# Performance work log

Hardware: AMD Instinct MI355X
Metric: run time of the kernel (lower is better)

## Reference

```python
import jax, jax.numpy as jnp
import numpy as np
from jax import lax

GRID_SIZE = 5
SPLINE_ORDER = 3
N_COEF = GRID_SIZE + SPLINE_ORDER  # 8 b-spline basis functions per input
GRID_LO, GRID_HI = -1.0, 1.0


def _grid():
    h = (GRID_HI - GRID_LO) / GRID_SIZE
    return jnp.arange(-SPLINE_ORDER, GRID_SIZE + SPLINE_ORDER + 1, dtype=jnp.float32) * h + GRID_LO


def _bsplines(x):
    # x: [..., in] -> [..., in, N_COEF] via Cox-de Boor recursion (efficient-kan)
    grid = _grid()
    x = x[..., None]
    bases = ((x >= grid[:-1]) & (x < grid[1:])).astype(x.dtype)
    for j in range(1, SPLINE_ORDER + 1):
        bases = ((x - grid[:-(j + 1)]) / (grid[j:-1] - grid[:-(j + 1)]) * bases[..., :-1]
                 + (grid[j + 1:] - x) / (grid[j + 1:] - grid[1:-j]) * bases[..., 1:])
    return bases


def _kan_linear(x, base_w, spline_w):
    # x: [..., in]; base_w: [out, in]; spline_w: [out, in, N_COEF]
    base = jax.nn.silu(x) @ base_w.T
    b = _bsplines(x).reshape(x.shape[:-1] + (-1,))  # [..., in*N_COEF]
    return base + b @ spline_w.reshape(spline_w.shape[0], -1).T


def _kan_conv(x, base_w, spline_w):
    # x: [B, C, H, W]; 3x3 valid KAN convolution
    patches = lax.conv_general_dilated_patches(x, (3, 3), (1, 1), 'VALID')  # [B, C*9, H-2, W-2]
    p = patches.transpose(0, 2, 3, 1)  # [B, Ho, Wo, C*9]
    out = _kan_linear(p, base_w, spline_w)  # [B, Ho, Wo, out]
    return out.transpose(0, 3, 1, 2)


def _maxpool2(x):
    return lax.reduce_window(x, -jnp.inf, lax.max, (1, 1, 2, 2), (1, 1, 2, 2), 'VALID')


def setup_inputs() -> dict:
    key = jax.random.key(0)
    ks = jax.random.split(key, 12)
    B = 2048
    x = jax.random.uniform(ks[0], (B, 1, 28, 28), dtype=jnp.float32)
    s = 0.1
    return {
        'x': x,
        'bw1': jax.random.normal(ks[1], (5, 9), dtype=jnp.float32) * s,
        'sw1': jax.random.normal(ks[2], (5, 9, N_COEF), dtype=jnp.float32) * s,
        'bw2': jax.random.normal(ks[3], (5, 45), dtype=jnp.float32) * s,
        'sw2': jax.random.normal(ks[4], (5, 45, N_COEF), dtype=jnp.float32) * s,
        'bw3': jax.random.normal(ks[5], (2, 45), dtype=jnp.float32) * s,
        'sw3': jax.random.normal(ks[6], (2, 45, N_COEF), dtype=jnp.float32) * s,
        'w1': jax.random.normal(ks[7], (500, 162), dtype=jnp.float32) * 0.05,
        'b1': jnp.zeros((500,), dtype=jnp.float32),
        'w2': jax.random.normal(ks[8], (10, 500), dtype=jnp.float32) * 0.05,
        'b2': jnp.zeros((10,), dtype=jnp.float32),
    }


def reference(x, bw1, sw1, bw2, sw2, bw3, sw3, w1, b1, w2, b2):
    h = _kan_conv(x, bw1, sw1)       # [B, 5, 26, 26]
    h = _maxpool2(h)                 # [B, 5, 13, 13]
    h = _kan_conv(h, bw2, sw2)       # [B, 5, 11, 11]
    h = _kan_conv(h, bw3, sw3)       # [B, 2, 9, 9]
    h = h.reshape(h.shape[0], -1)    # [B, 162]
    h = jax.nn.relu(h @ w1.T + b1)   # [B, 500]
    return h @ w2.T + b2             # [B, 10]
```

## Files before the change

### kernel.cpp

```cpp
#include <hip/hip_runtime.h>


typedef _Float16 h2 __attribute__((ext_vector_type(2)));

__device__ __forceinline__ h2 u2h(unsigned int u) {
  union { unsigned int x; h2 h; } v; v.x = u; return v.h;
}
__device__ __forceinline__ unsigned short f2h_bits(float x) {
  union { _Float16 h; unsigned short u; } v; v.h = (_Float16)x; return v.u;
}
__device__ __forceinline__ float h2f(unsigned short u) {
  union { unsigned short u; _Float16 h; } v; v.u = u; return (float)v.h;
}
__device__ __forceinline__ unsigned int pack2h(float a, float b) {
  return (unsigned int)f2h_bits(a) | ((unsigned int)f2h_bits(b) << 16);
}
__device__ __forceinline__ float fdot2(h2 a, h2 b, float c) {
  return __builtin_amdgcn_fdot2(a, b, c, false);
}

__device__ __forceinline__ void featurize_regs(float v, uint4& bs, float& silu) {
  silu = v / (1.0f + __expf(-v));
  bs.x = 0u; bs.y = 0u; bs.z = 0u; bs.w = 0u;
  float u = fmaf(v, 2.5f, 5.5f);
  if (u >= 0.0f && u < 11.0f) {
    float tf = floorf(u);
    float f = u - tf, f2 = f * f, f3 = f2 * f, om = 1.0f - f;
    const float c6 = 1.0f / 6.0f;
    float w0 = om * om * om * c6;
    float w1 = (3.0f * f3 - 6.0f * f2 + 4.0f) * c6;
    float w2 = (-3.0f * f3 + 3.0f * f2 + 3.0f * f + 1.0f) * c6;
    float w3 = f3 * c6;
    unsigned long long w01 =
        (unsigned long long)f2h_bits(w0) |
        ((unsigned long long)f2h_bits(w1) << 16) |
        ((unsigned long long)f2h_bits(w2) << 32) |
        ((unsigned long long)f2h_bits(w3) << 48);
    int t = (int)tf;
    int s = 16 * t - 48;
    unsigned long long lo, hi;
    if (s >= 0) {
      lo = (s < 64) ? (w01 << s) : 0ull;
      hi = (s == 0) ? 0ull : ((s < 64) ? (w01 >> (64 - s)) : (w01 << (s - 64)));
    } else {
      lo = w01 >> (-s);
      hi = 0ull;
    }
    bs.x = (unsigned int)lo; bs.y = (unsigned int)(lo >> 32);
    bs.z = (unsigned int)hi; bs.w = (unsigned int)(hi >> 32);
  }
}

__global__ __launch_bounds__(256) void k_prep(
    const float* __restrict__ bw1, const float* __restrict__ sw1,
    const float* __restrict__ bw2, const float* __restrict__ sw2,
    const float* __restrict__ bw3, const float* __restrict__ sw3,
    const float* __restrict__ w1, const float* __restrict__ w2,
    unsigned int* __restrict__ V1s, float* __restrict__ V1b,
    unsigned int* __restrict__ V2s, float* __restrict__ V2b,
    unsigned int* __restrict__ V3s, float* __restrict__ V3b,
    unsigned int* __restrict__ W1p4, float* __restrict__ W2p) {
  int t = blockIdx.x * 256 + threadIdx.x;
  if (t < 180) {
    int p = t & 3, o = (t >> 2) % 5, in = t / 20;
    V1s[t] = pack2h(sw1[(o * 9 + in) * 8 + 2 * p], sw1[(o * 9 + in) * 8 + 2 * p + 1]);
  }
  if (t < 45)  { int o = t % 5, in = t / 5; V1b[t] = bw1[o * 9 + in]; }
  if (t < 900) {
    int p = t & 3, o = (t >> 2) % 5, in = t / 20;
    V2s[t] = pack2h(sw2[(o * 45 + in) * 8 + 2 * p], sw2[(o * 45 + in) * 8 + 2 * p + 1]);
  }
  if (t < 225) { int o = t % 5, in = t / 5; V2b[t] = bw2[o * 45 + in]; }
  if (t < 360) {
    int p = t & 3, o = (t >> 2) & 1, in = t / 8;
    V3s[t] = pack2h(sw3[(o * 45 + in) * 8 + 2 * p], sw3[(o * 45 + in) * 8 + 2 * p + 1]);
  }
  if (t < 90)  { int o = t % 2, in = t / 2; V3b[t] = bw3[o * 45 + in]; }
  if (t < 43008) {
    int j = t & 3, o = (t >> 2) & 511, g = t >> 11;
    int kp = g * 4 + j;
    W1p4[t] = (o < 500 && kp < 81)
                  ? pack2h(w1[o * 162 + 2 * kp], w1[o * 162 + 2 * kp + 1])
                  : 0u;
  }
  if (t < 5120) {
    int o = t >> 9, k = t & 511;
    W2p[t] = (k < 500) ? w2[o * 500 + k] : 0.0f;
  }
}

__global__ __launch_bounds__(128, 4) void k_fused(
    const float* __restrict__ x,
    const unsigned int* __restrict__ V1s, const float* __restrict__ V1b,
    const unsigned int* __restrict__ V2s, const float* __restrict__ V2b,
    const unsigned int* __restrict__ V3s, const float* __restrict__ V3b,
    const unsigned int* __restrict__ W1p4, const float* __restrict__ W2p,
    const float* __restrict__ b1, const float* __restrict__ b2,
    float* __restrict__ out) {
  __shared__ uint4 bas[845];
  __shared__ unsigned short slu16[848];
  __shared__ float red[20];
  float*        basF = (float*)bas;
  float*        h3f  = basF + 2048;
  unsigned int* hpk  = (unsigned int*)basF + 2560;
  const int b = blockIdx.x;
  const int tid = threadIdx.x;

  #pragma unroll 1
  for (int l = tid; l < 784; l += 128) {
    uint4 bs; float sl;
    featurize_regs(x[b * 784 + l], bs, sl);
    bas[l] = bs; slu16[l] = f2h_bits(sl);
  }
  __syncthreads();

  float h1v[2][5];
  #pragma unroll 1
  for (int it = 0; it < 2; ++it) {
    int p = it * 128 + tid;
    if (p < 169) {
      int py = p / 13, px = p % 13;
      int r0 = py * 2, c0 = px * 2;
      float wacc[4][5];
      #pragma unroll
      for (int wi = 0; wi < 4; ++wi)
        #pragma unroll
        for (int o = 0; o < 5; ++o) wacc[wi][o] = 0.0f;
      #pragma unroll
      for (int r = 0; r < 4; ++r) {
        uint4 q[4]; float sl[4];
        #pragma unroll
        for (int c = 0; c < 4; ++c) {
          q[c]  = bas[(r0 + r) * 28 + c0 + c];
          sl[c] = h2f(slu16[(r0 + r) * 28 + c0 + c]);
        }
        #pragma unroll
        for (int c = 0; c < 4; ++c) {
          h2 a0 = u2h(q[c].x), a1 = u2h(q[c].y), a2 = u2h(q[c].z), a3 = u2h(q[c].w);
          #pragma unroll
          for (int dy = 0; dy < 2; ++dy) {
            #pragma unroll
            for (int dx = 0; dx < 2; ++dx) {
              int ky = r - dy, kx = c - dx;
              if (ky >= 0 && ky < 3 && kx >= 0 && kx < 3) {
                const unsigned int* wp = V1s + (ky * 3 + kx) * 20;
                const float* bp = V1b + (ky * 3 + kx) * 5;
                #pragma unroll
                for (int o = 0; o < 5; ++o) {
                  float acc = wacc[dy * 2 + dx][o];
                  acc = fdot2(a0, u2h(wp[o * 4 + 0]), acc);
                  acc = fdot2(a1, u2h(wp[o * 4 + 1]), acc);
                  acc = fdot2(a2, u2h(wp[o * 4 + 2]), acc);
                  acc = fdot2(a3, u2h(wp[o * 4 + 3]), acc);
                  wacc[dy * 2 + dx][o] = fmaf(sl[c], bp[o], acc);
                }
              }
            }
          }
        }
      }
      #pragma unroll
      for (int o = 0; o < 5; ++o)
        h1v[it][o] = fmaxf(fmaxf(wacc[0][o], wacc[1][o]),
                           fmaxf(wacc[2][o], wacc[3][o]));
    }
  }
  __syncthreads();
  #pragma unroll 1
  for (int it = 0; it < 2; ++it) {
    int p = it * 128 + tid;
    if (p < 169) {
      #pragma unroll
      for (int o = 0; o < 5; ++o) {
        uint4 bs; float sl;
        featurize_regs(h1v[it][o], bs, sl);
        bas[o * 169 + p] = bs; slu16[o * 169 + p] = f2h_bits(sl);
      }
    }
  }
  __syncthreads();

  float acc2[5];
  {
    #pragma unroll
    for (int o = 0; o < 5; ++o) acc2[o] = 0.0f;
    int pc = (tid < 121) ? tid : 120;
    int y0 = pc / 11, x0 = pc % 11;
    #pragma unroll 1
    for (int cky = 0; cky < 15; ++cky) {
      int c = cky / 3, ky = cky - c * 3;
      int ba0 = c * 169 + (y0 + ky) * 13 + x0;
      uint4 q00 = bas[ba0], q01 = bas[ba0 + 1], q02 = bas[ba0 + 2];
      float s00 = h2f(slu16[ba0]), s01 = h2f(slu16[ba0 + 1]), s02 = h2f(slu16[ba0 + 2]);
      uint4 wq[15]; float wb[15];
      const uint4* wp4 = (const uint4*)(V2s + cky * 60);
      const float* bp  = V2b + cky * 15;
      #pragma unroll
      for (int i = 0; i < 15; ++i) { wq[i] = wp4[i]; wb[i] = bp[i]; }
      #pragma unroll
      for (int kx = 0; kx < 3; ++kx) {
        uint4 q = (kx == 0) ? q00 : ((kx == 1) ? q01 : q02);
        float sl = (kx == 0) ? s00 : ((kx == 1) ? s01 : s02);
        h2 a0 = u2h(q.x), a1 = u2h(q.y), a2 = u2h(q.z), a3 = u2h(q.w);
        #pragma unroll
        for (int o = 0; o < 5; ++o) {
          uint4 w = wq[kx * 5 + o];
          float a = acc2[o];
          a = fdot2(a0, u2h(w.x), a);
          a = fdot2(a1, u2h(w.y), a);
          a = fdot2(a2, u2h(w.z), a);
          a = fdot2(a3, u2h(w.w), a);
          acc2[o] = fmaf(sl, wb[kx * 5 + o], a);
        }
      }
    }
  }
  __syncthreads();
  if (tid < 121) {
    #pragma unroll
    for (int o = 0; o < 5; ++o) {
      uint4 bs; float sl;
      featurize_regs(acc2[o], bs, sl);
      bas[o * 121 + tid] = bs; slu16[o * 121 + tid] = f2h_bits(sl);
    }
  }
  __syncthreads();

  float acc3[2];
  {
    acc3[0] = acc3[1] = 0.0f;
    int pc = (tid < 81) ? tid : 80;
    int y0 = pc / 9, x0 = pc % 9;
    #pragma unroll 1
    for (int cky = 0; cky < 15; ++cky) {
      int c = cky / 3, ky = cky - c * 3;
      int ba0 = c * 121 + (y0 + ky) * 11 + x0;
      uint4 q00 = bas[ba0], q01 = bas[ba0 + 1], q02 = bas[ba0 + 2];
      float s00 = h2f(slu16[ba0]), s01 = h2f(slu16[ba0 + 1]), s02 = h2f(slu16[ba0 + 2]);
      uint4 wq[6]; float wb[6];
      const uint4* wp4 = (const uint4*)(V3s + cky * 24);
      const float* bp  = V3b + cky * 6;
      #pragma unroll
      for (int i = 0; i < 6; ++i) { wq[i] = wp4[i]; wb[i] = bp[i]; }
      #pragma unroll
      for (int kx = 0; kx < 3; ++kx) {
        uint4 q = (kx == 0) ? q00 : ((kx == 1) ? q01 : q02);
        float sl = (kx == 0) ? s00 : ((kx == 1) ? s01 : s02);
        h2 a0 = u2h(q.x), a1 = u2h(q.y), a2 = u2h(q.z), a3 = u2h(q.w);
        #pragma unroll
        for (int o = 0; o < 2; ++o) {
          uint4 w = wq[kx * 2 + o];
          float a = acc3[o];
          a = fdot2(a0, u2h(w.x), a);
          a = fdot2(a1, u2h(w.y), a);
          a = fdot2(a2, u2h(w.z), a);
          a = fdot2(a3, u2h(w.w), a);
          acc3[o] = fmaf(sl, wb[kx * 2 + o], a);
        }
      }
    }
  }
  __syncthreads();
  if (tid < 81) { h3f[tid] = acc3[0]; h3f[81 + tid] = acc3[1]; }
  __syncthreads();
  if (tid < 84)
    hpk[tid] = (tid < 81) ? pack2h(h3f[2 * tid], h3f[2 * tid + 1]) : 0u;
  __syncthreads();

  float fa[4];
  #pragma unroll
  for (int i = 0; i < 4; ++i) fa[i] = 0.0f;
  {
    const uint4* hp4 = (const uint4*)hpk;
    const uint4* wbase = (const uint4*)W1p4 + tid;
    uint4 wA[4], wB[4];
    #pragma unroll
    for (int i = 0; i < 4; ++i) wA[i] = wbase[i * 128];
    #pragma unroll 1
    for (int g = 0; g < 21; g += 2) {
      if (g + 1 < 21) {
        const uint4* p = wbase + (g + 1) * 512;
        #pragma unroll
        for (int i = 0; i < 4; ++i) wB[i] = p[i * 128];
      }
      {
        uint4 hk = hp4[g];
        #pragma unroll
        for (int i = 0; i < 4; ++i) {
          float a = fa[i];
          a = fdot2(u2h(hk.x), u2h(wA[i].x), a);
          a = fdot2(u2h(hk.y), u2h(wA[i].y), a);
          a = fdot2(u2h(hk.z), u2h(wA[i].z), a);
          a = fdot2(u2h(hk.w), u2h(wA[i].w), a);
          fa[i] = a;
        }
      }
      if (g + 2 < 21) {
        const uint4* p = wbase + (g + 2) * 512;
        #pragma unroll
        for (int i = 0; i < 4; ++i) wA[i] = p[i * 128];
      }
      if (g + 1 < 21) {
        uint4 hk = hp4[g + 1];
        #pragma unroll
        for (int i = 0; i < 4; ++i) {
          float a = fa[i];
          a = fdot2(u2h(hk.x), u2h(wB[i].x), a);
          a = fdot2(u2h(hk.y), u2h(wB[i].y), a);
          a = fdot2(u2h(hk.z), u2h(wB[i].z), a);
          a = fdot2(u2h(hk.w), u2h(wB[i].w), a);
          fa[i] = a;
        }
      }
    }
  }
  #pragma unroll
  for (int i = 0; i < 4; ++i) {
    int o = tid + 128 * i;
    float bb = (o < 500) ? b1[o] : 0.0f;
    float v = fa[i] + bb;
    basF[o] = (v > 0.0f && o < 500) ? v : 0.0f;
  }
  __syncthreads();

  float acc10[10];
  {
    float4 ha = ((const float4*)basF)[tid];
    #pragma unroll
    for (int o = 0; o < 10; ++o) {
      const float4* wp = (const float4*)&W2p[o * 512 + 4 * tid];
      float4 w = wp[0];
      acc10[o] = ha.x * w.x + ha.y * w.y + ha.z * w.z + ha.w * w.w;
    }
  }
  #pragma unroll
  for (int off = 32; off > 0; off >>= 1) {
    #pragma unroll
    for (int o = 0; o < 10; ++o) acc10[o] += __shfl_down(acc10[o], off);
  }
  if ((tid & 63) == 0) {
    int wid = tid >> 6;
    #pragma unroll
    for (int o = 0; o < 10; ++o) red[wid * 10 + o] = acc10[o];
  }
  __syncthreads();
  if (tid < 10) out[b * 10 + tid] = red[tid] + red[10 + tid] + b2[tid];
}

extern "C" void kernel_launch(void* const* d_in, const int* in_sizes, int n_in,
                              void* d_out, int out_size, void* d_ws, size_t ws_size,
                              hipStream_t stream) {
  (void)in_sizes; (void)n_in; (void)out_size; (void)ws_size;
  const float* x   = (const float*)d_in[0];
  const float* bw1 = (const float*)d_in[1];
  const float* sw1 = (const float*)d_in[2];
  const float* bw2 = (const float*)d_in[3];
  const float* sw2 = (const float*)d_in[4];
  const float* bw3 = (const float*)d_in[5];
  const float* sw3 = (const float*)d_in[6];
  const float* w1  = (const float*)d_in[7];
  const float* b1  = (const float*)d_in[8];
  const float* w2  = (const float*)d_in[9];
  const float* b2  = (const float*)d_in[10];
  float* out = (float*)d_out;

  char* ws = (char*)d_ws;
  unsigned int* V1s  = (unsigned int*)(ws);
  float*        V1b  = (float*)(ws + 768);
  unsigned int* V2s  = (unsigned int*)(ws + 1024);
  float*        V2b  = (float*)(ws + 4672);
  unsigned int* V3s  = (unsigned int*)(ws + 5632);
  float*        V3b  = (float*)(ws + 7168);
  float*        W2p  = (float*)(ws + 7680);
  unsigned int* W1p4 = (unsigned int*)(ws + 28672);

  k_prep<<<168, 256, 0, stream>>>(bw1, sw1, bw2, sw2, bw3, sw3, w1, w2,
                                  V1s, V1b, V2s, V2b, V3s, V3b, W1p4, W2p);
  k_fused<<<2048, 128, 0, stream>>>(x, V1s, V1b, V2s, V2b, V3s, V3b,
                                    W1p4, W2p, b1, b2, out);
}
```

Baseline: 127.9 us.

## Double block size to 256 threads and split output channels across wave halves

Raises the fused per-sample block from 128 to 256 threads. Conv1 now gives each of the 169 pooled positions its own thread instead of looping twice. In conv2 and conv3 the two 128-thread halves split the output channels (3/2 for conv2, 1/1 for conv3), and the dense layers spread the 512 outputs and the final reduction over 4 waves. The aim is shorter per-thread serial chains and more parallel work per sample. In exchange, more threads sit idle in tail phases and launch bounds are tightened to 256x8, which may pressure registers.

```diff
diff --git a/kernel.cpp b/kernel.cpp
--- a/kernel.cpp
+++ b/kernel.cpp
@@ -51,6 +51,46 @@
   }
 }
 
+template <int OB, int NO>
+__device__ __forceinline__ void conv2_accum(
+    const uint4* bas, const unsigned short* slu16,
+    const unsigned int* __restrict__ V2s, const float* __restrict__ V2b,
+    int y0, int x0, float (&acc)[NO]) {
+  #pragma unroll 1
+  for (int cky = 0; cky < 15; ++cky) {
+    int c = cky / 3, ky = cky - c * 3;
+    int ba0 = c * 169 + (y0 + ky) * 13 + x0;
+    uint4 q00 = bas[ba0], q01 = bas[ba0 + 1], q02 = bas[ba0 + 2];
+    float s00 = h2f(slu16[ba0]), s01 = h2f(slu16[ba0 + 1]), s02 = h2f(slu16[ba0 + 2]);
+    uint4 wq[3 * NO]; float wb[3 * NO];
+    const uint4* wp4 = (const uint4*)(V2s + cky * 60);
+    const float* bp  = V2b + cky * 15;
+    #pragma unroll
+    for (int kx = 0; kx < 3; ++kx)
+      #pragma unroll
+      for (int j = 0; j < NO; ++j) {
+        wq[kx * NO + j] = wp4[kx * 5 + OB + j];
+        wb[kx * NO + j] = bp[kx * 5 + OB + j];
+      }
+    #pragma unroll
+    for (int kx = 0; kx < 3; ++kx) {
+      uint4 q = (kx == 0) ? q00 : ((kx == 1) ? q01 : q02);
+      float sl = (kx == 0) ? s00 : ((kx == 1) ? s01 : s02);
+      h2 a0 = u2h(q.x), a1 = u2h(q.y), a2 = u2h(q.z), a3 = u2h(q.w);
+      #pragma unroll
+      for (int j = 0; j < NO; ++j) {
+        uint4 w = wq[kx * NO + j];
+        float a = acc[j];
+        a = fdot2(a0, u2h(w.x), a);
+        a = fdot2(a1, u2h(w.y), a);
+        a = fdot2(a2, u2h(w.z), a);
+        a = fdot2(a3, u2h(w.w), a);
+        acc[j] = fmaf(sl, wb[kx * NO + j], a);
+      }
+    }
+  }
+}
+
 __global__ __launch_bounds__(256) void k_prep(
     const float* __restrict__ bw1, const float* __restrict__ sw1,
     const float* __restrict__ bw2, const float* __restrict__ sw2,
@@ -89,7 +129,7 @@
   }
 }
 
-__global__ __launch_bounds__(128, 4) void k_fused(
+__global__ __launch_bounds__(256, 8) void k_fused(
     const float* __restrict__ x,
     const unsigned int* __restrict__ V1s, const float* __restrict__ V1b,
     const unsigned int* __restrict__ V2s, const float* __restrict__ V2b,
@@ -99,7 +139,7 @@
     float* __restrict__ out) {
   __shared__ uint4 bas[845];
   __shared__ unsigned short slu16[848];
-  __shared__ float red[20];
+  __shared__ float red[40];
   float*        basF = (float*)bas;
   float*        h3f  = basF + 2048;
   unsigned int* hpk  = (unsigned int*)basF + 2560;
@@ -107,129 +147,105 @@
   const int tid = threadIdx.x;
 
   #pragma unroll 1
-  for (int l = tid; l < 784; l += 128) {
+  for (int l = tid; l < 784; l += 256) {
     uint4 bs; float sl;
     featurize_regs(x[b * 784 + l], bs, sl);
     bas[l] = bs; slu16[l] = f2h_bits(sl);
   }
   __syncthreads();
 
-  float h1v[2][5];
-  #pragma unroll 1
-  for (int it = 0; it < 2; ++it) {
-    int p = it * 128 + tid;
-    if (p < 169) {
-      int py = p / 13, px = p % 13;
-      int r0 = py * 2, c0 = px * 2;
-      float wacc[4][5];
-      #pragma unroll
-      for (int wi = 0; wi < 4; ++wi)
-        #pragma unroll
-        for (int o = 0; o < 5; ++o) wacc[wi][o] = 0.0f;
-      #pragma unroll
-      for (int r = 0; r < 4; ++r) {
-        uint4 q[4]; float sl[4];
-        #pragma unroll
-        for (int c = 0; c < 4; ++c) {
-          q[c]  = bas[(r0 + r) * 28 + c0 + c];
-          sl[c] = h2f(slu16[(r0 + r) * 28 + c0 + c]);
-        }
-        #pragma unroll
-        for (int c = 0; c < 4; ++c) {
-          h2 a0 = u2h(q[c].x), a1 = u2h(q[c].y), a2 = u2h(q[c].z), a3 = u2h(q[c].w);
+  float h1v[5];
+  if (tid < 169) {
+    int py = tid / 13, px = tid % 13;
+    int r0 = py * 2, c0 = px * 2;
+    float wacc[4][5];
+    #pragma unroll
+    for (int wi = 0; wi < 4; ++wi)
+      #pragma unroll
+      for (int o = 0; o < 5; ++o) wacc[wi][o] = 0.0f;
+    #pragma unroll
+    for (int r = 0; r < 4; ++r) {
+      uint4 q[4]; float sl[4];
+      #pragma unroll
+      for (int c = 0; c < 4; ++c) {
+        q[c]  = bas[(r0 + r) * 28 + c0 + c];
+        sl[c] = h2f(slu16[(r0 + r) * 28 + c0 + c]);
+      }
+      #pragma unroll
+      for (int c = 0; c < 4; ++c) {
+        h2 a0 = u2h(q[c].x), a1 = u2h(q[c].y), a2 = u2h(q[c].z), a3 = u2h(q[c].w);
+        #pragma unroll
+        for (int dy = 0; dy < 2; ++dy) {
           #pragma unroll
-          for (int dy = 0; dy < 2; ++dy) {
-            #pragma unroll
-            for (int dx = 0; dx < 2; ++dx) {
-              int ky = r - dy, kx = c - dx;
-              if (ky >= 0 && ky < 3 && kx >= 0 && kx < 3) {
-                const unsigned int* wp = V1s + (ky * 3 + kx) * 20;
-                const float* bp = V1b + (ky * 3 + kx) * 5;
-                #pragma unroll
-                for (int o = 0; o < 5; ++o) {
-                  float acc = wacc[dy * 2 + dx][o];
-                  acc = fdot2(a0, u2h(wp[o * 4 + 0]), acc);
-                  acc = fdot2(a1, u2h(wp[o * 4 + 1]), acc);
-                  acc = fdot2(a2, u2h(wp[o * 4 + 2]), acc);
-                  acc = fdot2(a3, u2h(wp[o * 4 + 3]), acc);
-                  wacc[dy * 2 + dx][o] = fmaf(sl[c], bp[o], acc);
-                }
+          for (int dx = 0; dx < 2; ++dx) {
+            int ky = r - dy, kx = c - dx;
+            if (ky >= 0 && ky < 3 && kx >= 0 && kx < 3) {
+              const unsigned int* wp = V1s + (ky * 3 + kx) * 20;
+              const float* bp = V1b + (ky * 3 + kx) * 5;
+              #pragma unroll
+              for (int o = 0; o < 5; ++o) {
+                float acc = wacc[dy * 2 + dx][o];
+                acc = fdot2(a0, u2h(wp[o * 4 + 0]), acc);
+                acc = fdot2(a1, u2h(wp[o * 4 + 1]), acc);
+                acc = fdot2(a2, u2h(wp[o * 4 + 2]), acc);
+                acc = fdot2(a3, u2h(wp[o * 4 + 3]), acc);
+                wacc[dy * 2 + dx][o] = fmaf(sl[c], bp[o], acc);
               }
             }
           }
         }
       }
-      #pragma unroll
-      for (int o = 0; o < 5; ++o)
-        h1v[it][o] = fmaxf(fmaxf(wacc[0][o], wacc[1][o]),
-                           fmaxf(wacc[2][o], wacc[3][o]));
-    }
-  }
-  __syncthreads();
-  #pragma unroll 1
-  for (int it = 0; it < 2; ++it) {
-    int p = it * 128 + tid;
-    if (p < 169) {
-      #pragma unroll
-      for (int o = 0; o < 5; ++o) {
-        uint4 bs; float sl;
-        featurize_regs(h1v[it][o], bs, sl);
-        bas[o * 169 + p] = bs; slu16[o * 169 + p] = f2h_bits(sl);
-      }
-    }
-  }
-  __syncthreads();
-
-  float acc2[5];
-  {
-    #pragma unroll
-    for (int o = 0; o < 5; ++o) acc2[o] = 0.0f;
-    int pc = (tid < 121) ? tid : 120;
-    int y0 = pc / 11, x0 = pc % 11;
-    #pragma unroll 1
-    for (int cky = 0; cky < 15; ++cky) {
-      int c = cky / 3, ky = cky - c * 3;
-      int ba0 = c * 169 + (y0 + ky) * 13 + x0;
-      uint4 q00 = bas[ba0], q01 = bas[ba0 + 1], q02 = bas[ba0 + 2];
-      float s00 = h2f(slu16[ba0]), s01 = h2f(slu16[ba0 + 1]), s02 = h2f(slu16[ba0 + 2]);
-      uint4 wq[15]; float wb[15];
-      const uint4* wp4 = (const uint4*)(V2s + cky * 60);
-      const float* bp  = V2b + cky * 15;
-      #pragma unroll
-      for (int i = 0; i < 15; ++i) { wq[i] = wp4[i]; wb[i] = bp[i]; }
-      #pragma unroll
-      for (int kx = 0; kx < 3; ++kx) {
-        uint4 q = (kx == 0) ? q00 : ((kx == 1) ? q01 : q02);
-        float sl = (kx == 0) ? s00 : ((kx == 1) ? s01 : s02);
-        h2 a0 = u2h(q.x), a1 = u2h(q.y), a2 = u2h(q.z), a3 = u2h(q.w);
-        #pragma unroll
-        for (int o = 0; o < 5; ++o) {
-          uint4 w = wq[kx * 5 + o];
-          float a = acc2[o];
-          a = fdot2(a0, u2h(w.x), a);
-          a = fdot2(a1, u2h(w.y), a);
-          a = fdot2(a2, u2h(w.z), a);
-          a = fdot2(a3, u2h(w.w), a);
-          acc2[o] = fmaf(sl, wb[kx * 5 + o], a);
-        }
-      }
-    }
-  }
-  __syncthreads();
-  if (tid < 121) {
+    }
+    #pragma unroll
+    for (int o = 0; o < 5; ++o)
+      h1v[o] = fmaxf(fmaxf(wacc[0][o], wacc[1][o]),
+                     fmaxf(wacc[2][o], wacc[3][o]));
+  }
+  __syncthreads();
+  if (tid < 169) {
     #pragma unroll
     for (int o = 0; o < 5; ++o) {
       uint4 bs; float sl;
-      featurize_regs(acc2[o], bs, sl);
-      bas[o * 121 + tid] = bs; slu16[o * 121 + tid] = f2h_bits(sl);
-    }
-  }
-  __syncthreads();
-
-  float acc3[2];
+      featurize_regs(h1v[o], bs, sl);
+      bas[o * 169 + tid] = bs; slu16[o * 169 + tid] = f2h_bits(sl);
+    }
+  }
+  __syncthreads();
+
+  int og = __builtin_amdgcn_readfirstlane(tid >> 7);
+  int p2 = tid & 127;
+  float acc2a[3] = {0.0f, 0.0f, 0.0f};
+  float acc2b[2] = {0.0f, 0.0f};
   {
-    acc3[0] = acc3[1] = 0.0f;
-    int pc = (tid < 81) ? tid : 80;
+    int pc = (p2 < 121) ? p2 : 120;
+    int y0 = pc / 11, x0 = pc % 11;
+    if (og == 0) conv2_accum<0, 3>(bas, slu16, V2s, V2b, y0, x0, acc2a);
+    else         conv2_accum<3, 2>(bas, slu16, V2s, V2b, y0, x0, acc2b);
+  }
+  __syncthreads();
+  if (p2 < 121) {
+    if (og == 0) {
+      #pragma unroll
+      for (int j = 0; j < 3; ++j) {
+        uint4 bs; float sl;
+        featurize_regs(acc2a[j], bs, sl);
+        bas[j * 121 + p2] = bs; slu16[j * 121 + p2] = f2h_bits(sl);
+      }
+    } else {
+      #pragma unroll
+      for (int j = 0; j < 2; ++j) {
+        uint4 bs; float sl;
+        featurize_regs(acc2b[j], bs, sl);
+        bas[(3 + j) * 121 + p2] = bs; slu16[(3 + j) * 121 + p2] = f2h_bits(sl);
+      }
+    }
+  }
+  __syncthreads();
+
+  float acc3 = 0.0f;
+  {
+    int ou = og;
+    int pc = (p2 < 81) ? p2 : 80;
     int y0 = pc / 9, x0 = pc % 9;
     #pragma unroll 1
     for (int cky = 0; cky < 15; ++cky) {
@@ -237,56 +253,54 @@
       int ba0 = c * 121 + (y0 + ky) * 11 + x0;
       uint4 q00 = bas[ba0], q01 = bas[ba0 + 1], q02 = bas[ba0 + 2];
       float s00 = h2f(slu16[ba0]), s01 = h2f(slu16[ba0 + 1]), s02 = h2f(slu16[ba0 + 2]);
-      uint4 wq[6]; float wb[6];
+      uint4 wq[3]; float wb[3];
       const uint4* wp4 = (const uint4*)(V3s + cky * 24);
       const float* bp  = V3b + cky * 6;
       #pragma unroll
-      for (int i = 0; i < 6; ++i) { wq[i] = wp4[i]; wb[i] = bp[i]; }
+      for (int kx = 0; kx < 3; ++kx) {
+        wq[kx] = wp4[kx * 2 + ou];
+        wb[kx] = bp[kx * 2 + ou];
+      }
       #pragma unroll
       for (int kx = 0; kx < 3; ++kx) {
         uint4 q = (kx == 0) ? q00 : ((kx == 1) ? q01 : q02);
         float sl = (kx == 0) ? s00 : ((kx == 1) ? s01 : s02);
         h2 a0 = u2h(q.x), a1 = u2h(q.y), a2 = u2h(q.z), a3 = u2h(q.w);
-        #pragma unroll
-        for (int o = 0; o < 2; ++o) {
-          uint4 w = wq[kx * 2 + o];
-          float a = acc3[o];
-          a = fdot2(a0, u2h(w.x), a);
-          a = fdot2(a1, u2h(w.y), a);
-          a = fdot2(a2, u2h(w.z), a);
-          a = fdot2(a3, u2h(w.w), a);
-          acc3[o] = fmaf(sl, wb[kx * 2 + o], a);
-        }
-      }
-    }
-  }
-  __syncthreads();
-  if (tid < 81) { h3f[tid] = acc3[0]; h3f[81 + tid] = acc3[1]; }
+        uint4 w = wq[kx];
+        float a = acc3;
+        a = fdot2(a0, u2h(w.x), a);
+        a = fdot2(a1, u2h(w.y), a);
+        a = fdot2(a2, u2h(w.z), a);
+        a = fdot2(a3, u2h(w.w), a);
+        acc3 = fmaf(sl, wb[kx], a);
+      }
+    }
+  }
+  __syncthreads();
+  if (p2 < 81) h3f[og * 81 + p2] = acc3;
   __syncthreads();
   if (tid < 84)
     hpk[tid] = (tid < 81) ? pack2h(h3f[2 * tid], h3f[2 * tid + 1]) : 0u;
   __syncthreads();
 
-  float fa[4];
-  #pragma unroll
-  for (int i = 0; i < 4; ++i) fa[i] = 0.0f;
+  float fa[2] = {0.0f, 0.0f};
   {
     const uint4* hp4 = (const uint4*)hpk;
     const uint4* wbase = (const uint4*)W1p4 + tid;
-    uint4 wA[4], wB[4];
-    #pragma unroll
-    for (int i = 0; i < 4; ++i) wA[i] = wbase[i * 128];
+    uint4 wA[2], wB[2];
+    #pragma unroll
+    for (int i = 0; i < 2; ++i) wA[i] = wbase[i * 256];
     #pragma unroll 1
     for (int g = 0; g < 21; g += 2) {
       if (g + 1 < 21) {
         const uint4* p = wbase + (g + 1) * 512;
         #pragma unroll
-        for (int i = 0; i < 4; ++i) wB[i] = p[i * 128];
+        for (int i = 0; i < 2; ++i) wB[i] = p[i * 256];
       }
       {
         uint4 hk = hp4[g];
         #pragma unroll
-        for (int i = 0; i < 4; ++i) {
+        for (int i = 0; i < 2; ++i) {
           float a = fa[i];
           a = fdot2(u2h(hk.x), u2h(wA[i].x), a);
           a = fdot2(u2h(hk.y), u2h(wA[i].y), a);
@@ -298,12 +312,12 @@
       if (g + 2 < 21) {
         const uint4* p = wbase + (g + 2) * 512;
         #pragma unroll
-        for (int i = 0; i < 4; ++i) wA[i] = p[i * 128];
+        for (int i = 0; i < 2; ++i) wA[i] = p[i * 256];
       }
       if (g + 1 < 21) {
         uint4 hk = hp4[g + 1];
         #pragma unroll
-        for (int i = 0; i < 4; ++i) {
+        for (int i = 0; i < 2; ++i) {
           float a = fa[i];
           a = fdot2(u2h(hk.x), u2h(wB[i].x), a);
           a = fdot2(u2h(hk.y), u2h(wB[i].y), a);
@@ -315,8 +329,8 @@
     }
   }
   #pragma unroll
-  for (int i = 0; i < 4; ++i) {
-    int o = tid + 128 * i;
+  for (int i = 0; i < 2; ++i) {
+    int o = tid + 256 * i;
     float bb = (o < 500) ? b1[o] : 0.0f;
     float v = fa[i] + bb;
     basF[o] = (v > 0.0f && o < 500) ? v : 0.0f;
@@ -325,12 +339,11 @@
 
   float acc10[10];
   {
-    float4 ha = ((const float4*)basF)[tid];
+    float2 ha = ((const float2*)basF)[tid];
     #pragma unroll
     for (int o = 0; o < 10; ++o) {
-      const float4* wp = (const float4*)&W2p[o * 512 + 4 * tid];
-      float4 w = wp[0];
-      acc10[o] = ha.x * w.x + ha.y * w.y + ha.z * w.z + ha.w * w.w;
+      float2 w = ((const float2*)&W2p[o * 512])[tid];
+      acc10[o] = ha.x * w.x + ha.y * w.y;
     }
   }
   #pragma unroll
@@ -344,7 +357,8 @@
     for (int o = 0; o < 10; ++o) red[wid * 10 + o] = acc10[o];
   }
   __syncthreads();
-  if (tid < 10) out[b * 10 + tid] = red[tid] + red[10 + tid] + b2[tid];
+  if (tid < 10)
+    out[b * 10 + tid] = red[tid] + red[10 + tid] + red[20 + tid] + red[30 + tid] + b2[tid];
 }
 
 extern "C" void kernel_launch(void* const* d_in, const int* in_sizes, int n_in,
@@ -376,6 +390,6 @@
 
   k_prep<<<168, 256, 0, stream>>>(bw1, sw1, bw2, sw2, bw3, sw3, w1, w2,
                                   V1s, V1b, V2s, V2b, V3s, V3b, W1p4, W2p);
-  k_fused<<<2048, 128, 0, stream>>>(x, V1s, V1b, V2s, V2b, V3s, V3b,
+  k_fused<<<2048, 256, 0, stream>>>(x, V1s, V1b, V2s, V2b, V3s, V3b,
                                     W1p4, W2p, b1, b2, out);
 }
```

Result: no change. 129.1 us (+0.9%).
